# Performance work log

Hardware: AMD Instinct MI355X
Metric: run time of the kernel (lower is better)

## Reference

```python
import jax, jax.numpy as jnp
import numpy as np
from jax import lax


def _binarize(t):
    # sign binarization to +1/-1 (zero maps to -1, matching torch.where(t > 0, 1, -1))
    return jnp.where(t > 0, 1.0, -1.0).astype(t.dtype)


def _bconv(x, w, b):
    # binary conv: binarize input and weights, then standard 3x3 'same' conv
    y = lax.conv_general_dilated(
        _binarize(x), _binarize(w),
        window_strides=(1, 1), padding=((1, 1), (1, 1)),
        dimension_numbers=('NCHW', 'OIHW', 'NCHW'))
    return y + b[None, :, None, None]


def _maxpool2(x):
    return lax.reduce_window(x, -jnp.inf, lax.max, (1, 1, 2, 2), (1, 1, 2, 2), 'VALID')


def setup_inputs() -> dict:
    key = jax.random.key(0)
    ks = jax.random.split(key, 13)
    s = 0.1
    return {
        'x': jax.random.normal(ks[0], (4096, 1, 28, 28), jnp.float32),
        'w1': jax.random.normal(ks[1], (32, 1, 3, 3), jnp.float32) * s,
        'b1': jax.random.normal(ks[2], (32,), jnp.float32) * s,
        'w2': jax.random.normal(ks[3], (64, 32, 3, 3), jnp.float32) * s,
        'b2': jax.random.normal(ks[4], (64,), jnp.float32) * s,
        'w3': jax.random.normal(ks[5], (16, 64, 3, 3), jnp.float32) * s,
        'b3': jax.random.normal(ks[6], (16,), jnp.float32) * s,
        'fc1_w': jax.random.normal(ks[7], (256, 16 * 7 * 7), jnp.float32) * s,
        'fc1_b': jax.random.normal(ks[8], (256,), jnp.float32) * s,
        'fc2_w': jax.random.normal(ks[9], (128, 256), jnp.float32) * s,
        'fc2_b': jax.random.normal(ks[10], (128,), jnp.float32) * s,
        'fc3_w': jax.random.normal(ks[11], (10, 128), jnp.float32) * s,
        'fc3_b': jax.random.normal(ks[12], (10,), jnp.float32) * s,
    }


def reference(x, w1, b1, w2, b2, w3, b3, fc1_w, fc1_b, fc2_w, fc2_b, fc3_w, fc3_b):
    h = jax.nn.relu(_maxpool2(_bconv(x, w1, b1)))      # [B,32,14,14]
    h = jax.nn.relu(_maxpool2(_bconv(h, w2, b2)))      # [B,64,7,7]
    h = jax.nn.relu(_bconv(h, w3, b3))                 # [B,16,7,7]
    h = h.reshape(-1, 16 * 7 * 7)
    h = jax.nn.relu(h @ fc1_w.T + fc1_b)
    h = jax.nn.relu(h @ fc2_w.T + fc2_b)
    return h @ fc3_w.T + fc3_b                          # [B,10]
```

## Files before the change

### kernel.cpp

```cpp
#include <hip/hip_runtime.h>
#include <cstdint>

__global__ void pack_weights(const float* __restrict__ w1,
                             const float* __restrict__ w2,
                             const float* __restrict__ w3,
                             uint32_t* __restrict__ pw) {
    int t = threadIdx.x;
    if (t < 32) {
        uint32_t b = 0;
        for (int k = 0; k < 9; ++k) b |= (w1[t * 9 + k] > 0.f ? 1u : 0u) << k;
        pw[t] = b;
    }
    for (int idx = t; idx < 576; idx += blockDim.x) {
        int oc = idx / 9, tap = idx % 9;
        int kh = tap / 3, kw = tap % 3;
        uint32_t b = 0;
        for (int ic = 0; ic < 32; ++ic)
            b |= (w2[((oc * 32 + ic) * 3 + kh) * 3 + kw] > 0.f ? 1u : 0u) << ic;
        pw[32 + idx] = b;
    }
    for (int idx = t; idx < 144; idx += blockDim.x) {
        int oc = idx / 9, tap = idx % 9;
        int kh = tap / 3, kw = tap % 3;
        uint32_t lo = 0, hi = 0;
        for (int ic = 0; ic < 32; ++ic) {
            lo |= (w3[((oc * 64 + ic) * 3 + kh) * 3 + kw] > 0.f ? 1u : 0u) << ic;
            hi |= (w3[((oc * 64 + ic + 32) * 3 + kh) * 3 + kw] > 0.f ? 1u : 0u) << ic;
        }
        pw[608 + idx * 2] = lo;
        pw[608 + idx * 2 + 1] = hi;
    }
}

__global__ __launch_bounds__(256) void conv_stack(
    const float* __restrict__ x,
    const float* __restrict__ b1,
    const float* __restrict__ b2,
    const float* __restrict__ b3,
    const uint32_t* __restrict__ pw,
    float* __restrict__ h3g) {
    __shared__ uint32_t s_wb1[32];
    __shared__ uint32_t s_W2[576];
    __shared__ uint32_t s_W3[288];
    __shared__ float s_b1[32], s_b2[64], s_b3[16];
    __shared__ uint32_t s_xrow[28];
    __shared__ uint32_t s_H1[196];
    __shared__ uint32_t s_H2[98];

    const int t = threadIdx.x;
    const int img = blockIdx.x;

    if (t < 32) { s_wb1[t] = pw[t]; s_b1[t] = b1[t]; }
    if (t >= 32 && t < 96) s_b2[t - 32] = b2[t - 32];
    if (t >= 96 && t < 112) s_b3[t - 96] = b3[t - 96];
    for (int i = t; i < 576; i += 256) s_W2[i] = pw[32 + i];
    for (int i = t; i < 288; i += 256) s_W3[i] = pw[608 + i];
    if (t < 98) s_H2[t] = 0;
    if (t >= 128 && t < 156) {
        int r = t - 128;
        const float* xr = x + img * 784 + r * 28;
        uint32_t b = 0;
        for (int j = 0; j < 28; ++j) b |= (xr[j] > 0.f ? 1u : 0u) << j;
        s_xrow[r] = b;
    }
    __syncthreads();

    if (t < 196) {
        int pi = t / 14, pj = t % 14;
        uint32_t sarr[4], marr[4];
        int pcm[4];
#pragma unroll
        for (int p = 0; p < 4; ++p) {
            int i = 2 * pi + (p >> 1), j = 2 * pj + (p & 1);
            uint32_t sb = 0, mb = 0;
            int bit = 0;
#pragma unroll
            for (int di = -1; di <= 1; ++di) {
                int y = i + di;
                bool rv = (y >= 0 && y < 28);
                uint32_t row = rv ? s_xrow[y] : 0u;
#pragma unroll
                for (int dj = -1; dj <= 1; ++dj) {
                    int xx = j + dj;
                    bool v = rv && xx >= 0 && xx < 28;
                    if (v) {
                        mb |= 1u << bit;
                        sb |= ((row >> xx) & 1u) << bit;
                    }
                    ++bit;
                }
            }
            sarr[p] = sb; marr[p] = mb; pcm[p] = __popc(mb);
        }
        uint32_t word = 0;
#pragma unroll
        for (int c = 0; c < 32; ++c) {
            uint32_t w = s_wb1[c];
            int best = -100;
#pragma unroll
            for (int p = 0; p < 4; ++p) {
                int v = pcm[p] - 2 * __popc((sarr[p] ^ w) & marr[p]);
                best = v > best ? v : best;
            }
            word |= ((float)best + s_b1[c] > 0.f ? 1u : 0u) << c;
        }
        s_H1[t] = word;
    }
    __syncthreads();

    for (int task = t; task < 784; task += 256) {
        int quad = task / 49, pos = task % 49;
        int pi = pos / 7, pj = pos % 7;
        uint32_t cell[16];
        uint32_t vm = 0;
#pragma unroll
        for (int r = 0; r < 4; ++r) {
            int y = 2 * pi - 1 + r;
#pragma unroll
            for (int c = 0; c < 4; ++c) {
                int xx = 2 * pj - 1 + c;
                bool v = (y >= 0 && y < 14 && xx >= 0 && xx < 14);
                cell[r * 4 + c] = v ? s_H1[y * 14 + xx] : 0u;
                vm |= (v ? 1u : 0u) << (r * 4 + c);
            }
        }
        uint32_t nib = 0;
#pragma unroll
        for (int o = 0; o < 4; ++o) {
            int oc = quad * 4 + o;
            const uint32_t* wrow = &s_W2[oc * 9];
            int best = -10000;
#pragma unroll
            for (int p = 0; p < 4; ++p) {
                int a = p >> 1, b = p & 1;
                int acc = 0;
#pragma unroll
                for (int tap = 0; tap < 9; ++tap) {
                    int ci = (a + tap / 3) * 4 + (b + tap % 3);
                    int contrib = 32 - 2 * __popc(cell[ci] ^ wrow[tap]);
                    acc += ((vm >> ci) & 1u) ? contrib : 0;
                }
                best = acc > best ? acc : best;
            }
            nib |= ((float)best + s_b2[oc] > 0.f ? 1u : 0u) << (oc & 31);
        }
        atomicOr((unsigned int*)&s_H2[pos * 2 + (quad >> 3)], (unsigned int)nib);
    }
    __syncthreads();

    for (int task = t; task < 784; task += 256) {
        int oc = task / 49, pos = task % 49;
        int pi = pos / 7, pj = pos % 7;
        const uint32_t* wr = &s_W3[oc * 18];
        int acc = 0;
#pragma unroll
        for (int tap = 0; tap < 9; ++tap) {
            int y = pi + tap / 3 - 1, xx = pj + tap % 3 - 1;
            if (y >= 0 && y < 7 && xx >= 0 && xx < 7) {
                uint32_t lo = s_H2[(y * 7 + xx) * 2];
                uint32_t hi = s_H2[(y * 7 + xx) * 2 + 1];
                acc += 64 - 2 * (__popc(lo ^ wr[tap * 2]) + __popc(hi ^ wr[tap * 2 + 1]));
            }
        }
        float h = (float)acc + s_b3[oc];
        h3g[img * 784 + oc * 49 + pos] = h > 0.f ? h : 0.f;
    }
}

__global__ __launch_bounds__(256) void fc_stack(
    const float* __restrict__ h3g,
    const float* __restrict__ fc1_w, const float* __restrict__ fc1_b,
    const float* __restrict__ fc2_w, const float* __restrict__ fc2_b,
    const float* __restrict__ fc3_w, const float* __restrict__ fc3_b,
    float* __restrict__ out) {
    __shared__ __align__(16) float smem[784 * 20];
    float* s_h = smem;
    float* s_o1 = smem;
    float* s_part = smem + 256 * 20;
    float* s_o2 = smem + 256 * 20 + 256 * 16;

    const int t = threadIdx.x;
    const int ib = blockIdx.x * 16;

    for (int idx = t; idx < 16 * 784; idx += 256) {
        int i = idx / 784, k = idx % 784;
        s_h[k * 20 + i] = h3g[(ib + i) * 784 + k];
    }
    __syncthreads();

    float acc[16];
#pragma unroll
    for (int i = 0; i < 16; ++i) acc[i] = 0.f;
    {
        const float4* wrow = (const float4*)(fc1_w + t * 784);
        for (int k4 = 0; k4 < 196; ++k4) {
            float4 w = wrow[k4];
            float wv[4] = {w.x, w.y, w.z, w.w};
#pragma unroll
            for (int j = 0; j < 4; ++j) {
                const float4* h4 = (const float4*)(s_h + (k4 * 4 + j) * 20);
#pragma unroll
                for (int q = 0; q < 4; ++q) {
                    float4 hv = h4[q];
                    acc[q * 4 + 0] += wv[j] * hv.x;
                    acc[q * 4 + 1] += wv[j] * hv.y;
                    acc[q * 4 + 2] += wv[j] * hv.z;
                    acc[q * 4 + 3] += wv[j] * hv.w;
                }
            }
        }
    }
    float bn1 = fc1_b[t];
    __syncthreads();
#pragma unroll
    for (int i = 0; i < 16; ++i) {
        float v = acc[i] + bn1;
        s_o1[t * 20 + i] = v > 0.f ? v : 0.f;
    }
    __syncthreads();

    {
        int n = t & 127, half = t >> 7;
#pragma unroll
        for (int i = 0; i < 16; ++i) acc[i] = 0.f;
        const float4* wrow = (const float4*)(fc2_w + n * 256 + half * 128);
        for (int k4 = 0; k4 < 32; ++k4) {
            float4 w = wrow[k4];
            float wv[4] = {w.x, w.y, w.z, w.w};
#pragma unroll
            for (int j = 0; j < 4; ++j) {
                const float4* h4 = (const float4*)(s_o1 + (half * 128 + k4 * 4 + j) * 20);
#pragma unroll
                for (int q = 0; q < 4; ++q) {
                    float4 hv = h4[q];
                    acc[q * 4 + 0] += wv[j] * hv.x;
                    acc[q * 4 + 1] += wv[j] * hv.y;
                    acc[q * 4 + 2] += wv[j] * hv.z;
                    acc[q * 4 + 3] += wv[j] * hv.w;
                }
            }
        }
#pragma unroll
        for (int i = 0; i < 16; ++i) s_part[(half * 128 + n) * 16 + i] = acc[i];
    }
    __syncthreads();

    for (int idx = t; idx < 128 * 16; idx += 256) {
        int n = idx / 16, i = idx % 16;
        float v = s_part[n * 16 + i] + s_part[(128 + n) * 16 + i] + fc2_b[n];
        s_o2[n * 20 + i] = v > 0.f ? v : 0.f;
    }
    __syncthreads();

    if (t < 160) {
        int i = t / 10, n = t % 10;
        float a3 = fc3_b[n];
        const float* wr = fc3_w + n * 128;
        for (int k = 0; k < 128; ++k) a3 += wr[k] * s_o2[k * 20 + i];
        out[(ib + i) * 10 + n] = a3;
    }
}

extern "C" void kernel_launch(void* const* d_in, const int* in_sizes, int n_in,
                              void* d_out, int out_size, void* d_ws, size_t ws_size,
                              hipStream_t stream) {
    const float* x     = (const float*)d_in[0];
    const float* w1    = (const float*)d_in[1];
    const float* b1    = (const float*)d_in[2];
    const float* w2    = (const float*)d_in[3];
    const float* b2    = (const float*)d_in[4];
    const float* w3    = (const float*)d_in[5];
    const float* b3    = (const float*)d_in[6];
    const float* fc1_w = (const float*)d_in[7];
    const float* fc1_b = (const float*)d_in[8];
    const float* fc2_w = (const float*)d_in[9];
    const float* fc2_b = (const float*)d_in[10];
    const float* fc3_w = (const float*)d_in[11];
    const float* fc3_b = (const float*)d_in[12];
    float* out = (float*)d_out;

    const int B = in_sizes[0] / 784;

    uint32_t* pw = (uint32_t*)d_ws;
    float* h3g = (float*)((char*)d_ws + 4096);

    hipLaunchKernelGGL(pack_weights, dim3(1), dim3(256), 0, stream, w1, w2, w3, pw);
    hipLaunchKernelGGL(conv_stack, dim3(B), dim3(256), 0, stream,
                       x, b1, b2, b3, pw, h3g);
    hipLaunchKernelGGL(fc_stack, dim3(B / 16), dim3(256), 0, stream,
                       h3g, fc1_w, fc1_b, fc2_w, fc2_b, fc3_w, fc3_b, out);
}
```

Baseline: 258.8 us.

## Split FC stack into tiled transposed GEMMs and specialize conv2 interior/border

After: 220.1 us. 1.18x faster.

```diff
diff --git a/kernel.cpp b/kernel.cpp
--- a/kernel.cpp
+++ b/kernel.cpp
@@ -1,63 +1,83 @@
 #include <hip/hip_runtime.h>
 #include <cstdint>
 
-__global__ void pack_weights(const float* __restrict__ w1,
-                             const float* __restrict__ w2,
-                             const float* __restrict__ w3,
-                             uint32_t* __restrict__ pw) {
+#define OFF_PW    0
+#define OFF_W1T   4096
+#define OFF_W2T   823296
+#define OFF_H3T   954368
+#define OFF_H1T   14061568
+#define OFF_H2T   18255872
+
+__global__ __launch_bounds__(256) void prep(
+    const float* __restrict__ w1, const float* __restrict__ w2,
+    const float* __restrict__ w3,
+    const float* __restrict__ fc1_w, const float* __restrict__ fc2_w,
+    uint32_t* __restrict__ pw, float* __restrict__ w1T, float* __restrict__ w2T) {
     int t = threadIdx.x;
-    if (t < 32) {
-        uint32_t b = 0;
-        for (int k = 0; k < 9; ++k) b |= (w1[t * 9 + k] > 0.f ? 1u : 0u) << k;
-        pw[t] = b;
-    }
-    for (int idx = t; idx < 576; idx += blockDim.x) {
-        int oc = idx / 9, tap = idx % 9;
-        int kh = tap / 3, kw = tap % 3;
-        uint32_t b = 0;
-        for (int ic = 0; ic < 32; ++ic)
-            b |= (w2[((oc * 32 + ic) * 3 + kh) * 3 + kw] > 0.f ? 1u : 0u) << ic;
-        pw[32 + idx] = b;
-    }
-    for (int idx = t; idx < 144; idx += blockDim.x) {
-        int oc = idx / 9, tap = idx % 9;
-        int kh = tap / 3, kw = tap % 3;
-        uint32_t lo = 0, hi = 0;
-        for (int ic = 0; ic < 32; ++ic) {
-            lo |= (w3[((oc * 64 + ic) * 3 + kh) * 3 + kw] > 0.f ? 1u : 0u) << ic;
-            hi |= (w3[((oc * 64 + ic + 32) * 3 + kh) * 3 + kw] > 0.f ? 1u : 0u) << ic;
-        }
-        pw[608 + idx * 2] = lo;
-        pw[608 + idx * 2 + 1] = hi;
+    if (blockIdx.x == 0) {
+        if (t < 32) {
+            uint32_t b = 0;
+            for (int k = 0; k < 9; ++k) b |= (w1[t * 9 + k] > 0.f ? 1u : 0u) << k;
+            pw[t] = b;
+        }
+        for (int idx = t; idx < 576; idx += 256) {
+            int oc = idx / 9, tap = idx % 9;
+            int kh = tap / 3, kw = tap % 3;
+            uint32_t b = 0;
+            for (int ic = 0; ic < 32; ++ic)
+                b |= (w2[((oc * 32 + ic) * 3 + kh) * 3 + kw] > 0.f ? 1u : 0u) << ic;
+            pw[32 + idx] = b;
+        }
+        for (int idx = t; idx < 144; idx += 256) {
+            int oc = idx / 9, tap = idx % 9;
+            int kh = tap / 3, kw = tap % 3;
+            uint32_t lo = 0, hi = 0;
+            for (int ic = 0; ic < 32; ++ic) {
+                lo |= (w3[((oc * 64 + ic) * 3 + kh) * 3 + kw] > 0.f ? 1u : 0u) << ic;
+                hi |= (w3[((oc * 64 + ic + 32) * 3 + kh) * 3 + kw] > 0.f ? 1u : 0u) << ic;
+            }
+            pw[608 + idx * 2] = lo;
+            pw[608 + idx * 2 + 1] = hi;
+        }
+    } else {
+        int e = (blockIdx.x - 1) * 256 + t;
+        if (e < 204800) {
+            int k = e >> 8, n = e & 255;
+            w1T[e] = (k < 784) ? fc1_w[n * 784 + k] : 0.f;
+        } else {
+            int e2 = e - 204800;
+            int k = e2 >> 7, n = e2 & 127;
+            w2T[e2] = fc2_w[n * 256 + k];
+        }
     }
 }
 
 __global__ __launch_bounds__(256) void conv_stack(
     const float* __restrict__ x,
-    const float* __restrict__ b1,
-    const float* __restrict__ b2,
+    const float* __restrict__ b1, const float* __restrict__ b2,
     const float* __restrict__ b3,
     const uint32_t* __restrict__ pw,
-    float* __restrict__ h3g) {
+    float* __restrict__ h3T) {
     __shared__ uint32_t s_wb1[32];
     __shared__ uint32_t s_W2[576];
     __shared__ uint32_t s_W3[288];
     __shared__ float s_b1[32], s_b2[64], s_b3[16];
     __shared__ uint32_t s_xrow[28];
-    __shared__ uint32_t s_H1[196];
-    __shared__ uint32_t s_H2[98];
+    __shared__ uint32_t s_H1[256];
+    __shared__ uint32_t s_H2[162];
 
     const int t = threadIdx.x;
     const int img = blockIdx.x;
 
+    s_H1[t] = 0;
+    if (t < 162) s_H2[t] = 0;
     if (t < 32) { s_wb1[t] = pw[t]; s_b1[t] = b1[t]; }
     if (t >= 32 && t < 96) s_b2[t - 32] = b2[t - 32];
     if (t >= 96 && t < 112) s_b3[t - 96] = b3[t - 96];
     for (int i = t; i < 576; i += 256) s_W2[i] = pw[32 + i];
     for (int i = t; i < 288; i += 256) s_W3[i] = pw[608 + i];
-    if (t < 98) s_H2[t] = 0;
-    if (t >= 128 && t < 156) {
-        int r = t - 128;
+    if (t >= 192 && t < 220) {
+        int r = t - 192;
         const float* xr = x + img * 784 + r * 28;
         uint32_t b = 0;
         for (int j = 0; j < 28; ++j) b |= (xr[j] > 0.f ? 1u : 0u) << j;
@@ -77,12 +97,12 @@
 #pragma unroll
             for (int di = -1; di <= 1; ++di) {
                 int y = i + di;
-                bool rv = (y >= 0 && y < 28);
-                uint32_t row = rv ? s_xrow[y] : 0u;
+                bool rv = (unsigned)y < 28u;
+                uint32_t row = rv ? s_xrow[rv ? y : 0] : 0u;
 #pragma unroll
                 for (int dj = -1; dj <= 1; ++dj) {
                     int xx = j + dj;
-                    bool v = rv && xx >= 0 && xx < 28;
+                    bool v = rv && (unsigned)xx < 28u;
                     if (v) {
                         mb |= 1u << bit;
                         sb |= ((row >> xx) & 1u) << bit;
@@ -96,7 +116,7 @@
 #pragma unroll
         for (int c = 0; c < 32; ++c) {
             uint32_t w = s_wb1[c];
-            int best = -100;
+            int best = -1000;
 #pragma unroll
             for (int p = 0; p < 4; ++p) {
                 int v = pcm[p] - 2 * __popc((sarr[p] ^ w) & marr[p]);
@@ -104,161 +124,254 @@
             }
             word |= ((float)best + s_b1[c] > 0.f ? 1u : 0u) << c;
         }
-        s_H1[t] = word;
+        s_H1[(pi + 1) * 16 + (pj + 1)] = word;
     }
     __syncthreads();
 
+    for (int task = t; task < 400; task += 256) {
+        int q = task / 25, ip = task - q * 25;
+        int pi = ip / 5 + 1, pj = ip % 5 + 1;
+        uint32_t cell[16];
+#pragma unroll
+        for (int r = 0; r < 4; ++r)
+#pragma unroll
+            for (int c = 0; c < 4; ++c)
+                cell[r * 4 + c] = s_H1[(2 * pi + r) * 16 + (2 * pj + c)];
+        uint32_t nib = 0;
+#pragma unroll
+        for (int o = 0; o < 4; ++o) {
+            int oc = q * 4 + o;
+            const uint32_t* wrow = &s_W2[oc * 9];
+            int best = -100000;
+#pragma unroll
+            for (int a = 0; a < 2; ++a)
+#pragma unroll
+                for (int b = 0; b < 2; ++b) {
+                    int S = 0;
+#pragma unroll
+                    for (int kh = 0; kh < 3; ++kh)
+#pragma unroll
+                        for (int kw = 0; kw < 3; ++kw)
+                            S += __popc(cell[(a + kh) * 4 + (b + kw)] ^ wrow[kh * 3 + kw]);
+                    int v = 288 - 2 * S;
+                    best = v > best ? v : best;
+                }
+            nib |= ((float)best + s_b2[oc] > 0.f ? 1u : 0u) << (oc & 31);
+        }
+        atomicOr((unsigned int*)&s_H2[((pi + 1) * 9 + (pj + 1)) * 2 + (q >> 3)],
+                 (unsigned int)nib);
+    }
+    for (int task = t; task < 384; task += 256) {
+        int q = task / 24, bp = task - q * 24;
+        int pi, pj;
+        if (bp < 7)       { pi = 0; pj = bp; }
+        else if (bp < 14) { pi = 6; pj = bp - 7; }
+        else if (bp < 19) { pi = bp - 13; pj = 0; }
+        else              { pi = bp - 18; pj = 6; }
+        uint32_t vr[4], vc[4];
+#pragma unroll
+        for (int r = 0; r < 4; ++r) {
+            vr[r] = ((unsigned)(2 * pi - 1 + r) < 14u) ? 0xFFFFFFFFu : 0u;
+            vc[r] = ((unsigned)(2 * pj - 1 + r) < 14u) ? 0xFFFFFFFFu : 0u;
+        }
+        uint32_t cell[16], V[16];
+#pragma unroll
+        for (int r = 0; r < 4; ++r)
+#pragma unroll
+            for (int c = 0; c < 4; ++c) {
+                cell[r * 4 + c] = s_H1[(2 * pi + r) * 16 + (2 * pj + c)];
+                V[r * 4 + c] = vr[r] & vc[c];
+            }
+        int nvp[4];
+#pragma unroll
+        for (int a = 0; a < 2; ++a)
+#pragma unroll
+            for (int b = 0; b < 2; ++b) {
+                int i = 2 * pi + a, j = 2 * pj + b;
+                int vy = 3 - (i == 0) - (i == 13);
+                int vx = 3 - (j == 0) - (j == 13);
+                nvp[a * 2 + b] = 32 * vy * vx;
+            }
+        uint32_t nib = 0;
+#pragma unroll
+        for (int o = 0; o < 4; ++o) {
+            int oc = q * 4 + o;
+            const uint32_t* wrow = &s_W2[oc * 9];
+            int best = -100000;
+#pragma unroll
+            for (int a = 0; a < 2; ++a)
+#pragma unroll
+                for (int b = 0; b < 2; ++b) {
+                    int S = 0;
+#pragma unroll
+                    for (int kh = 0; kh < 3; ++kh)
+#pragma unroll
+                        for (int kw = 0; kw < 3; ++kw) {
+                            int ci = (a + kh) * 4 + (b + kw);
+                            S += __popc((cell[ci] ^ wrow[kh * 3 + kw]) & V[ci]);
+                        }
+                    int v = nvp[a * 2 + b] - 2 * S;
+                    best = v > best ? v : best;
+                }
+            nib |= ((float)best + s_b2[oc] > 0.f ? 1u : 0u) << (oc & 31);
+        }
+        atomicOr((unsigned int*)&s_H2[((pi + 1) * 9 + (pj + 1)) * 2 + (q >> 3)],
+                 (unsigned int)nib);
+    }
+    __syncthreads();
+
     for (int task = t; task < 784; task += 256) {
-        int quad = task / 49, pos = task % 49;
+        int oc = task / 49, pos = task - oc * 49;
         int pi = pos / 7, pj = pos % 7;
-        uint32_t cell[16];
-        uint32_t vm = 0;
-#pragma unroll
-        for (int r = 0; r < 4; ++r) {
-            int y = 2 * pi - 1 + r;
-#pragma unroll
-            for (int c = 0; c < 4; ++c) {
-                int xx = 2 * pj - 1 + c;
-                bool v = (y >= 0 && y < 14 && xx >= 0 && xx < 14);
-                cell[r * 4 + c] = v ? s_H1[y * 14 + xx] : 0u;
-                vm |= (v ? 1u : 0u) << (r * 4 + c);
-            }
-        }
-        uint32_t nib = 0;
-#pragma unroll
-        for (int o = 0; o < 4; ++o) {
-            int oc = quad * 4 + o;
-            const uint32_t* wrow = &s_W2[oc * 9];
-            int best = -10000;
-#pragma unroll
-            for (int p = 0; p < 4; ++p) {
-                int a = p >> 1, b = p & 1;
-                int acc = 0;
-#pragma unroll
-                for (int tap = 0; tap < 9; ++tap) {
-                    int ci = (a + tap / 3) * 4 + (b + tap % 3);
-                    int contrib = 32 - 2 * __popc(cell[ci] ^ wrow[tap]);
-                    acc += ((vm >> ci) & 1u) ? contrib : 0;
-                }
-                best = acc > best ? acc : best;
-            }
-            nib |= ((float)best + s_b2[oc] > 0.f ? 1u : 0u) << (oc & 31);
-        }
-        atomicOr((unsigned int*)&s_H2[pos * 2 + (quad >> 3)], (unsigned int)nib);
-    }
-    __syncthreads();
-
-    for (int task = t; task < 784; task += 256) {
-        int oc = task / 49, pos = task % 49;
-        int pi = pos / 7, pj = pos % 7;
+        uint32_t vr[3], vc[3];
+#pragma unroll
+        for (int d = 0; d < 3; ++d) {
+            vr[d] = ((unsigned)(pi - 1 + d) < 7u) ? 0xFFFFFFFFu : 0u;
+            vc[d] = ((unsigned)(pj - 1 + d) < 7u) ? 0xFFFFFFFFu : 0u;
+        }
+        int vy = 3 - (pi == 0) - (pi == 6);
+        int vx = 3 - (pj == 0) - (pj == 6);
+        int Nv = 64 * vy * vx;
         const uint32_t* wr = &s_W3[oc * 18];
-        int acc = 0;
-#pragma unroll
-        for (int tap = 0; tap < 9; ++tap) {
-            int y = pi + tap / 3 - 1, xx = pj + tap % 3 - 1;
-            if (y >= 0 && y < 7 && xx >= 0 && xx < 7) {
-                uint32_t lo = s_H2[(y * 7 + xx) * 2];
-                uint32_t hi = s_H2[(y * 7 + xx) * 2 + 1];
-                acc += 64 - 2 * (__popc(lo ^ wr[tap * 2]) + __popc(hi ^ wr[tap * 2 + 1]));
-            }
-        }
-        float h = (float)acc + s_b3[oc];
-        h3g[img * 784 + oc * 49 + pos] = h > 0.f ? h : 0.f;
-    }
-}
-
-__global__ __launch_bounds__(256) void fc_stack(
-    const float* __restrict__ h3g,
-    const float* __restrict__ fc1_w, const float* __restrict__ fc1_b,
-    const float* __restrict__ fc2_w, const float* __restrict__ fc2_b,
-    const float* __restrict__ fc3_w, const float* __restrict__ fc3_b,
+        int S = 0;
+#pragma unroll
+        for (int kh = 0; kh < 3; ++kh)
+#pragma unroll
+            for (int kw = 0; kw < 3; ++kw) {
+                uint32_t V = vr[kh] & vc[kw];
+                int idx = ((pi + kh) * 9 + (pj + kw)) * 2;
+                S += __popc((s_H2[idx] ^ wr[(kh * 3 + kw) * 2]) & V);
+                S += __popc((s_H2[idx + 1] ^ wr[(kh * 3 + kw) * 2 + 1]) & V);
+            }
+        float h = (float)(Nv - 2 * S) + s_b3[oc];
+        h3T[task * 4096 + img] = h > 0.f ? h : 0.f;
+    }
+}
+
+__global__ __launch_bounds__(256) void fc1_gemm(
+    const float* __restrict__ aT,
+    const float* __restrict__ bT,
+    const float* __restrict__ bias,
+    float* __restrict__ oT) {
+    const int KC = 80, LD = 68;
+    __shared__ float As[KC * LD];
+    __shared__ float Bs[KC * LD];
+    const int t = threadIdx.x;
+    const int tx = t & 15, ty = t >> 4;
+    const int img0 = blockIdx.x * 64;
+    const int n0 = blockIdx.y * 64;
+    float acc[4][4] = {{0.f}};
+
+    for (int kc = 0; kc < 800; kc += KC) {
+#pragma unroll
+        for (int s = 0; s < 5; ++s) {
+            int v = t + s * 256;
+            int kk = v >> 4, i4 = (v & 15) * 4;
+            *(float4*)&As[kk * LD + i4] =
+                *(const float4*)&aT[(kc + kk) * 4096 + img0 + i4];
+            *(float4*)&Bs[kk * LD + i4] =
+                *(const float4*)&bT[(kc + kk) * 256 + n0 + i4];
+        }
+        __syncthreads();
+#pragma unroll 4
+        for (int kk = 0; kk < KC; ++kk) {
+            float4 a = *(const float4*)&As[kk * LD + ty * 4];
+            float4 b = *(const float4*)&Bs[kk * LD + tx * 4];
+            acc[0][0] += a.x * b.x; acc[0][1] += a.x * b.y;
+            acc[0][2] += a.x * b.z; acc[0][3] += a.x * b.w;
+            acc[1][0] += a.y * b.x; acc[1][1] += a.y * b.y;
+            acc[1][2] += a.y * b.z; acc[1][3] += a.y * b.w;
+            acc[2][0] += a.z * b.x; acc[2][1] += a.z * b.y;
+            acc[2][2] += a.z * b.z; acc[2][3] += a.z * b.w;
+            acc[3][0] += a.w * b.x; acc[3][1] += a.w * b.y;
+            acc[3][2] += a.w * b.z; acc[3][3] += a.w * b.w;
+        }
+        __syncthreads();
+    }
+    float4 bb = *(const float4*)&bias[n0 + tx * 4];
+    float bv[4] = {bb.x, bb.y, bb.z, bb.w};
+#pragma unroll
+    for (int jj = 0; jj < 4; ++jj) {
+        float4 ov;
+        ov.x = acc[0][jj] + bv[jj]; ov.x = ov.x > 0.f ? ov.x : 0.f;
+        ov.y = acc[1][jj] + bv[jj]; ov.y = ov.y > 0.f ? ov.y : 0.f;
+        ov.z = acc[2][jj] + bv[jj]; ov.z = ov.z > 0.f ? ov.z : 0.f;
+        ov.w = acc[3][jj] + bv[jj]; ov.w = ov.w > 0.f ? ov.w : 0.f;
+        *(float4*)&oT[(n0 + tx * 4 + jj) * 4096 + img0 + ty * 4] = ov;
+    }
+}
+
+__global__ __launch_bounds__(256) void fc2_gemm(
+    const float* __restrict__ aT,
+    const float* __restrict__ bT,
+    const float* __restrict__ bias,
+    float* __restrict__ oT) {
+    const int KC = 64, LDA = 68, LDB = 36;
+    __shared__ float As[KC * LDA];
+    __shared__ float Bs[KC * LDB];
+    const int t = threadIdx.x;
+    const int tx = t & 15, ty = t >> 4;
+    const int img0 = blockIdx.x * 64;
+    const int n0 = blockIdx.y * 32;
+    float acc[4][2] = {{0.f}};
+
+    for (int kc = 0; kc < 256; kc += KC) {
+#pragma unroll
+        for (int s = 0; s < 4; ++s) {
+            int v = t + s * 256;
+            int kk = v >> 4, i4 = (v & 15) * 4;
+            *(float4*)&As[kk * LDA + i4] =
+                *(const float4*)&aT[(kc + kk) * 4096 + img0 + i4];
+        }
+#pragma unroll
+        for (int s = 0; s < 2; ++s) {
+            int v = t + s * 256;
+            int kk = v >> 3, n4 = (v & 7) * 4;
+            *(float4*)&Bs[kk * LDB + n4] =
+                *(const float4*)&bT[(kc + kk) * 128 + n0 + n4];
+        }
+        __syncthreads();
+#pragma unroll 4
+        for (int kk = 0; kk < KC; ++kk) {
+            float4 a = *(const float4*)&As[kk * LDA + ty * 4];
+            float2 b = *(const float2*)&Bs[kk * LDB + tx * 2];
+            acc[0][0] += a.x * b.x; acc[0][1] += a.x * b.y;
+            acc[1][0] += a.y * b.x; acc[1][1] += a.y * b.y;
+            acc[2][0] += a.z * b.x; acc[2][1] += a.z * b.y;
+            acc[3][0] += a.w * b.x; acc[3][1] += a.w * b.y;
+        }
+        __syncthreads();
+    }
+#pragma unroll
+    for (int j = 0; j < 2; ++j) {
+        int n = n0 + tx * 2 + j;
+        float bj = bias[n];
+        float4 ov;
+        ov.x = acc[0][j] + bj; ov.x = ov.x > 0.f ? ov.x : 0.f;
+        ov.y = acc[1][j] + bj; ov.y = ov.y > 0.f ? ov.y : 0.f;
+        ov.z = acc[2][j] + bj; ov.z = ov.z > 0.f ? ov.z : 0.f;
+        ov.w = acc[3][j] + bj; ov.w = ov.w > 0.f ? ov.w : 0.f;
+        *(float4*)&oT[n * 4096 + img0 + ty * 4] = ov;
+    }
+}
+
+__global__ __launch_bounds__(256) void fc3_gemm(
+    const float* __restrict__ aT,
+    const float* __restrict__ w,
+    const float* __restrict__ bias,
     float* __restrict__ out) {
-    __shared__ __align__(16) float smem[784 * 20];
-    float* s_h = smem;
-    float* s_o1 = smem;
-    float* s_part = smem + 256 * 20;
-    float* s_o2 = smem + 256 * 20 + 256 * 16;
-
-    const int t = threadIdx.x;
-    const int ib = blockIdx.x * 16;
-
-    for (int idx = t; idx < 16 * 784; idx += 256) {
-        int i = idx / 784, k = idx % 784;
-        s_h[k * 20 + i] = h3g[(ib + i) * 784 + k];
-    }
-    __syncthreads();
-
-    float acc[16];
-#pragma unroll
-    for (int i = 0; i < 16; ++i) acc[i] = 0.f;
-    {
-        const float4* wrow = (const float4*)(fc1_w + t * 784);
-        for (int k4 = 0; k4 < 196; ++k4) {
-            float4 w = wrow[k4];
-            float wv[4] = {w.x, w.y, w.z, w.w};
-#pragma unroll
-            for (int j = 0; j < 4; ++j) {
-                const float4* h4 = (const float4*)(s_h + (k4 * 4 + j) * 20);
-#pragma unroll
-                for (int q = 0; q < 4; ++q) {
-                    float4 hv = h4[q];
-                    acc[q * 4 + 0] += wv[j] * hv.x;
-                    acc[q * 4 + 1] += wv[j] * hv.y;
-                    acc[q * 4 + 2] += wv[j] * hv.z;
-                    acc[q * 4 + 3] += wv[j] * hv.w;
-                }
-            }
-        }
-    }
-    float bn1 = fc1_b[t];
-    __syncthreads();
-#pragma unroll
-    for (int i = 0; i < 16; ++i) {
-        float v = acc[i] + bn1;
-        s_o1[t * 20 + i] = v > 0.f ? v : 0.f;
-    }
-    __syncthreads();
-
-    {
-        int n = t & 127, half = t >> 7;
-#pragma unroll
-        for (int i = 0; i < 16; ++i) acc[i] = 0.f;
-        const float4* wrow = (const float4*)(fc2_w + n * 256 + half * 128);
-        for (int k4 = 0; k4 < 32; ++k4) {
-            float4 w = wrow[k4];
-            float wv[4] = {w.x, w.y, w.z, w.w};
-#pragma unroll
-            for (int j = 0; j < 4; ++j) {
-                const float4* h4 = (const float4*)(s_o1 + (half * 128 + k4 * 4 + j) * 20);
-#pragma unroll
-                for (int q = 0; q < 4; ++q) {
-                    float4 hv = h4[q];
-                    acc[q * 4 + 0] += wv[j] * hv.x;
-                    acc[q * 4 + 1] += wv[j] * hv.y;
-                    acc[q * 4 + 2] += wv[j] * hv.z;
-                    acc[q * 4 + 3] += wv[j] * hv.w;
-                }
-            }
-        }
-#pragma unroll
-        for (int i = 0; i < 16; ++i) s_part[(half * 128 + n) * 16 + i] = acc[i];
-    }
-    __syncthreads();
-
-    for (int idx = t; idx < 128 * 16; idx += 256) {
-        int n = idx / 16, i = idx % 16;
-        float v = s_part[n * 16 + i] + s_part[(128 + n) * 16 + i] + fc2_b[n];
-        s_o2[n * 20 + i] = v > 0.f ? v : 0.f;
-    }
-    __syncthreads();
-
-    if (t < 160) {
-        int i = t / 10, n = t % 10;
-        float a3 = fc3_b[n];
-        const float* wr = fc3_w + n * 128;
-        for (int k = 0; k < 128; ++k) a3 += wr[k] * s_o2[k * 20 + i];
-        out[(ib + i) * 10 + n] = a3;
-    }
+    int id = blockIdx.x * 256 + threadIdx.x;
+    int n = id >> 12, img = id & 4095;
+    const float* wr = w + n * 128;
+    float a0 = 0.f, a1 = 0.f, a2 = 0.f, a3 = 0.f;
+#pragma unroll 8
+    for (int k = 0; k < 128; k += 4) {
+        a0 += aT[(k + 0) * 4096 + img] * wr[k + 0];
+        a1 += aT[(k + 1) * 4096 + img] * wr[k + 1];
+        a2 += aT[(k + 2) * 4096 + img] * wr[k + 2];
+        a3 += aT[(k + 3) * 4096 + img] * wr[k + 3];
+    }
+    out[img * 10 + n] = (a0 + a1) + (a2 + a3) + bias[n];
 }
 
 extern "C" void kernel_launch(void* const* d_in, const int* in_sizes, int n_in,
@@ -280,13 +393,22 @@
     float* out = (float*)d_out;
 
     const int B = in_sizes[0] / 784;
-
-    uint32_t* pw = (uint32_t*)d_ws;
-    float* h3g = (float*)((char*)d_ws + 4096);
-
-    hipLaunchKernelGGL(pack_weights, dim3(1), dim3(256), 0, stream, w1, w2, w3, pw);
+    char* ws = (char*)d_ws;
+    uint32_t* pw = (uint32_t*)(ws + OFF_PW);
+    float* w1T = (float*)(ws + OFF_W1T);
+    float* w2T = (float*)(ws + OFF_W2T);
+    float* h3T = (float*)(ws + OFF_H3T);
+    float* h1T = (float*)(ws + OFF_H1T);
+    float* h2T = (float*)(ws + OFF_H2T);
+
+    hipLaunchKernelGGL(prep, dim3(929), dim3(256), 0, stream,
+                       w1, w2, w3, fc1_w, fc2_w, pw, w1T, w2T);
     hipLaunchKernelGGL(conv_stack, dim3(B), dim3(256), 0, stream,
-                       x, b1, b2, b3, pw, h3g);
-    hipLaunchKernelGGL(fc_stack, dim3(B / 16), dim3(256), 0, stream,
-                       h3g, fc1_w, fc1_b, fc2_w, fc2_b, fc3_w, fc3_b, out);
-}
+                       x, b1, b2, b3, pw, h3T);
+    hipLaunchKernelGGL(fc1_gemm, dim3(B / 64, 4), dim3(256), 0, stream,
+                       h3T, w1T, fc1_b, h1T);
+    hipLaunchKernelGGL(fc2_gemm, dim3(B / 64, 4), dim3(256), 0, stream,
+                       h1T, w2T, fc2_b, h2T);
+    hipLaunchKernelGGL(fc3_gemm, dim3(B * 10 / 256), dim3(256), 0, stream,
+                       h2T, fc3_w, fc3_b, out);
+}
```
